# Performance work log

Hardware: AMD Instinct MI355X
Metric: run time of the kernel (lower is better)

The kernel has to match this reference:

```python
import jax, jax.numpy as jnp
import numpy as np

B = 64            # batch of graphs
E = 8978          # edge-simplices per graph (nodes of the Hodge-1 graph)
E2 = E // 2       # after Graclus pair-pooling
K = 4             # Laguerre polynomial order
DEG = 16          # avg degree of the (edge-)adjacency
SLOPE = 0.33      # LeakyReLU negative slope
EPS = 1e-5        # BatchNorm eps


def _make_edges(rng, b, n, deg):
    # block-diagonal batched edge list: each graph only connects within itself
    offs = np.repeat(np.arange(b, dtype=np.int64) * n, n * deg)
    dst = np.tile(np.repeat(np.arange(n, dtype=np.int64), deg), b) + offs
    src = rng.integers(0, n, size=b * n * deg) + offs
    return np.stack([src, dst]).astype(np.int32)


def setup_inputs() -> dict:
    rng = np.random.default_rng(0)
    ks = jax.random.split(jax.random.key(0), 12)
    N1 = B * E
    ei1 = _make_edges(rng, B, E, DEG)
    ei2 = _make_edges(rng, B, E2, DEG)
    return {
        "x_s": jax.random.normal(ks[0], (N1, 1), jnp.float32),
        "edge_index_s": jnp.asarray(ei1),
        "edge_weight_s": jax.random.uniform(ks[1], (ei1.shape[1],), jnp.float32) * (2.0 / DEG),
        "edge_index_s1": jnp.asarray(ei2),
        "edge_weight_s1": jax.random.uniform(ks[2], (ei2.shape[1],), jnp.float32) * (2.0 / DEG),
        "W0": jax.random.normal(ks[3], (K, 1, 32), jnp.float32) * 0.3,
        "b0": jnp.zeros((32,), jnp.float32),
        "g0": jnp.ones((32,), jnp.float32),
        "be0": jnp.zeros((32,), jnp.float32),
        "W1": jax.random.normal(ks[4], (K, 32, 32), jnp.float32) * 0.1,
        "b1": jnp.zeros((32,), jnp.float32),
        "g1": jnp.ones((32,), jnp.float32),
        "be1": jnp.zeros((32,), jnp.float32),
        "W2": jax.random.normal(ks[5], (K, 32, 1), jnp.float32) * 0.1,
        "b2": jnp.zeros((1,), jnp.float32),
        "g2": jnp.ones((1,), jnp.float32),
        "be2": jnp.zeros((1,), jnp.float32),
        "lin1_W": jax.random.normal(ks[6], (E2, 256), jnp.float32) * 0.02,
        "lin1_b": jnp.zeros((256,), jnp.float32),
        "bn1_g": jnp.ones((256,), jnp.float32),
        "bn1_b": jnp.zeros((256,), jnp.float32),
        "lin2_W": jax.random.normal(ks[7], (256, 128), jnp.float32) * 0.06,
        "lin2_b": jnp.zeros((128,), jnp.float32),
        "bn2_g": jnp.ones((128,), jnp.float32),
        "bn2_b": jnp.zeros((128,), jnp.float32),
        "lin3_W": jax.random.normal(ks[8], (128, 1), jnp.float32) * 0.09,
        "lin3_b": jnp.zeros((1,), jnp.float32),
    }


def _laguerre_layer(x, src, dst, ew, W, b, gamma, beta, n):
    """HodgeLaguerreConv (K-order Laguerre recurrence over sparse L) + BatchNorm + LeakyReLU."""
    def matvec(v):  # (L v)[i] = sum_j w_ij v[j]
        return jax.ops.segment_sum(ew[:, None] * v[src], dst, num_segments=n)
    Tp = x                      # L_0(L) x = x
    out = Tp @ W[0]
    Tc = x - matvec(x)          # L_1(L) x = x - L x
    out = out + Tc @ W[1]
    for k in range(1, K - 1):   # L_{k+1} = ((2k+1-L) L_k - k L_{k-1}) / (k+1)
        Tn = ((2 * k + 1) * Tc - matvec(Tc) - k * Tp) / (k + 1)
        out = out + Tn @ W[k + 1]
        Tp, Tc = Tc, Tn
    out = out + b
    out = gamma * (out - out.mean(0)) * jax.lax.rsqrt(out.var(0) + EPS) + beta
    return jnp.where(out > 0, out, SLOPE * out)


def _bn(h, g, b):
    return g * (h - h.mean(0)) * jax.lax.rsqrt(h.var(0) + EPS) + b


def reference(x_s, edge_index_s, edge_weight_s, edge_index_s1, edge_weight_s1,
              W0, b0, g0, be0, W1, b1, g1, be1, W2, b2, g2, be2,
              lin1_W, lin1_b, bn1_g, bn1_b, lin2_W, lin2_b, bn2_g, bn2_b,
              lin3_W, lin3_b):
    N1, N2 = B * E, B * E2
    x = _laguerre_layer(x_s, edge_index_s[0], edge_index_s[1], edge_weight_s,
                        W0, b0, g0, be0, N1)
    # Graclus pooling: merge matched node pairs by max over features
    x = x.reshape(B, E2, 2, x.shape[-1]).max(axis=2).reshape(N2, -1)
    x = _laguerre_layer(x, edge_index_s1[0], edge_index_s1[1], edge_weight_s1,
                        W1, b1, g1, be1, N2)
    x = _laguerre_layer(x, edge_index_s1[0], edge_index_s1[1], edge_weight_s1,
                        W2, b2, g2, be2, N2)
    x = x.reshape(B, E2)        # last conv has 1 channel
    h = jax.nn.relu(_bn(x @ lin1_W + lin1_b, bn1_g, bn1_b))
    h = jax.nn.relu(_bn(h @ lin2_W + lin2_b, bn2_g, bn2_b))
    return h @ lin3_W + lin3_b  # [B, num_classes=1]
```

## Files before the change

kernel.cpp:

```cpp
#include <hip/hip_runtime.h>
#include <cstdint>

#define SLOPE 0.33f

static constexpr int B_   = 64;
static constexpr int E1_  = 8978;
static constexpr int E2_  = 4489;
static constexpr int N1_  = B_ * E1_;
static constexpr int N2_  = B_ * E2_;
static constexpr int DEG_ = 16;
static constexpr int QTR_ = 2245;
static constexpr int QTR2_ = 1123;
static constexpr int MVGRID = (N2_ * 32) / 256;
static constexpr int PROJ_GRID = (N2_ + 511) / 512;
static constexpr double EPS_ = 1e-5;

__device__ __forceinline__ float lrelu(float v) { return v > 0.f ? v : SLOPE * v; }
__device__ __forceinline__ float dot4(float4 a, float4 b) {
  return a.x * b.x + a.y * b.y + a.z * b.z + a.w * b.w;
}

__global__ __launch_bounds__(1024) void k0_chain(const float* __restrict__ x,
    const int* __restrict__ src, const float* __restrict__ ew,
    float* __restrict__ T1, float* __restrict__ T2, float* __restrict__ T3,
    double* mom) {
  __shared__ float sx[E1_], s1[E1_], s2[E1_];
  __shared__ double sred[16][14];
  int v = (blockIdx.x & 7) * 32 + (blockIdx.x >> 3);
  int g = v >> 2, q = v & 3;
  int gbase = g * E1_;
  int tid = threadIdx.x;
  for (int i = tid; i < E1_; i += 1024) sx[i] = x[gbase + i];
  __syncthreads();
  for (int i = tid; i < E1_; i += 1024) {
    const int4* s4 = (const int4*)(src + (size_t)(gbase + i) * DEG_);
    const float4* w4 = (const float4*)(ew + (size_t)(gbase + i) * DEG_);
    float acc = 0.f;
#pragma unroll
    for (int j = 0; j < 4; ++j) {
      int4 s = s4[j]; float4 w = w4[j];
      acc += w.x * sx[s.x - gbase] + w.y * sx[s.y - gbase]
           + w.z * sx[s.z - gbase] + w.w * sx[s.w - gbase];
    }
    s1[i] = sx[i] - acc;
  }
  __syncthreads();
  for (int i = tid; i < E1_; i += 1024) {
    const int4* s4 = (const int4*)(src + (size_t)(gbase + i) * DEG_);
    const float4* w4 = (const float4*)(ew + (size_t)(gbase + i) * DEG_);
    float acc = 0.f;
#pragma unroll
    for (int j = 0; j < 4; ++j) {
      int4 s = s4[j]; float4 w = w4[j];
      acc += w.x * s1[s.x - gbase] + w.y * s1[s.y - gbase]
           + w.z * s1[s.z - gbase] + w.w * s1[s.w - gbase];
    }
    s2[i] = (3.f * s1[i] - acc - sx[i]) * 0.5f;
  }
  __syncthreads();
  double m[14];
#pragma unroll
  for (int j = 0; j < 14; ++j) m[j] = 0.0;
  int start = q * QTR_, end = min(start + QTR_, E1_);
  for (int i = start + tid; i < end; i += 1024) {
    const int4* s4 = (const int4*)(src + (size_t)(gbase + i) * DEG_);
    const float4* w4 = (const float4*)(ew + (size_t)(gbase + i) * DEG_);
    float acc = 0.f;
#pragma unroll
    for (int j = 0; j < 4; ++j) {
      int4 s = s4[j]; float4 w = w4[j];
      acc += w.x * s2[s.x - gbase] + w.y * s2[s.y - gbase]
           + w.z * s2[s.z - gbase] + w.w * s2[s.w - gbase];
    }
    float t1 = s1[i], t2 = s2[i];
    float t3 = (5.f * t2 - acc - 2.f * t1) * (1.f / 3.f);
    T1[gbase + i] = t1;
    T2[gbase + i] = t2;
    T3[gbase + i] = t3;
    double d0 = sx[i], d1 = t1, d2 = t2, d3 = t3;
    m[0] += d0; m[1] += d1; m[2] += d2; m[3] += d3;
    m[4] += d0 * d0; m[5] += d0 * d1; m[6] += d0 * d2; m[7] += d0 * d3;
    m[8] += d1 * d1; m[9] += d1 * d2; m[10] += d1 * d3;
    m[11] += d2 * d2; m[12] += d2 * d3; m[13] += d3 * d3;
  }
  int lane = tid & 63, wid = tid >> 6;
#pragma unroll
  for (int j = 0; j < 14; ++j) {
    double vv = m[j];
    for (int o = 32; o; o >>= 1) vv += __shfl_down(vv, o);
    if (lane == 0) sred[wid][j] = vv;
  }
  __syncthreads();
  if (tid < 14) {
    double s = 0.0;
#pragma unroll
    for (int w = 0; w < 16; ++w) s += sred[w][tid];
    atomicAdd(&mom[tid], s);
  }
}

__global__ void k0_params(const double* __restrict__ mom, const float* __restrict__ W0,
    const float* __restrict__ g0, const float* __restrict__ be0,
    float* __restrict__ scale0, float* __restrict__ shiftE0) {
  int c = threadIdx.x;
  if (c >= 32) return;
  double inv = 1.0 / (double)N1_;
  double mm[4];
#pragma unroll
  for (int k = 0; k < 4; ++k) mm[k] = mom[k] * inv;
  double M[4][4];
  M[0][0] = mom[4] * inv;  M[0][1] = mom[5] * inv;  M[0][2] = mom[6] * inv;  M[0][3] = mom[7] * inv;
  M[1][1] = mom[8] * inv;  M[1][2] = mom[9] * inv;  M[1][3] = mom[10] * inv;
  M[2][2] = mom[11] * inv; M[2][3] = mom[12] * inv; M[3][3] = mom[13] * inv;
  M[1][0] = M[0][1]; M[2][0] = M[0][2]; M[3][0] = M[0][3];
  M[2][1] = M[1][2]; M[3][1] = M[1][3]; M[3][2] = M[2][3];
  double w[4];
#pragma unroll
  for (int k = 0; k < 4; ++k) w[k] = W0[k * 32 + c];
  double mean = 0.0;
#pragma unroll
  for (int k = 0; k < 4; ++k) mean += w[k] * mm[k];
  double e2 = 0.0;
#pragma unroll
  for (int k = 0; k < 4; ++k)
#pragma unroll
    for (int l = 0; l < 4; ++l) e2 += M[k][l] * w[k] * w[l];
  double var = e2 - mean * mean;
  double sc = (double)g0[c] / sqrt(var + EPS_);
  scale0[c] = (float)sc;
  shiftE0[c] = (float)((double)be0[c] - sc * mean);
}

__global__ __launch_bounds__(256) void k0_pool(const float* __restrict__ x,
    const float* __restrict__ T1, const float* __restrict__ T2, const float* __restrict__ T3,
    const float* __restrict__ W0, const float* __restrict__ scale0,
    const float* __restrict__ shiftE0, float* __restrict__ x1) {
  int gid = blockIdx.x * 256 + threadIdx.x;
  int grp = gid >> 5, c = gid & 31;
  if (grp >= N2_) return;
  int b = grp / E2_, j = grp - b * E2_;
  int ga = b * E1_ + 2 * j, gb = ga + 1;
  float w0 = W0[c], w1 = W0[32 + c], w2 = W0[64 + c], w3 = W0[96 + c];
  float da = x[ga] * w0 + T1[ga] * w1 + T2[ga] * w2 + T3[ga] * w3;
  float db = x[gb] * w0 + T1[gb] * w1 + T2[gb] * w2 + T3[gb] * w3;
  float sc = scale0[c], sh = shiftE0[c];
  float ya = lrelu(sc * da + sh), yb = lrelu(sc * db + sh);
  x1[grp * 32 + c] = fmaxf(ya, yb);
}

__global__ __launch_bounds__(256) void k1_projall(const float* __restrict__ X,
    const float* __restrict__ W1, float4* __restrict__ P4) {
  __shared__ float4 Wl[128 * 8];
  const float4 cfs[4] = { {0.f, 0.f, 0.f, -1.f / 6.f},
                          {0.f, 0.f, 0.5f, 1.5f},
                          {0.f, -1.f, -2.f, -3.f},
                          {1.f, 1.f, 1.f, 1.f} };
  for (int e = threadIdx.x; e < 1024; e += 256) {
    int o = e >> 3, qq = e & 7;
    int j = o >> 5, cp = o & 31;
    float4 cf = cfs[j];
    float4 w;
    {
      const float* wp = W1 + (4 * qq + 0) * 32 + cp;
      w.x = cf.x * wp[0] + cf.y * wp[1024] + cf.z * wp[2048] + cf.w * wp[3072];
    }
    {
      const float* wp = W1 + (4 * qq + 1) * 32 + cp;
      w.y = cf.x * wp[0] + cf.y * wp[1024] + cf.z * wp[2048] + cf.w * wp[3072];
    }
    {
      const float* wp = W1 + (4 * qq + 2) * 32 + cp;
      w.z = cf.x * wp[0] + cf.y * wp[1024] + cf.z * wp[2048] + cf.w * wp[3072];
    }
    {
      const float* wp = W1 + (4 * qq + 3) * 32 + cp;
      w.w = cf.x * wp[0] + cf.y * wp[1024] + cf.z * wp[2048] + cf.w * wp[3072];
    }
    Wl[e] = w;
  }
  __syncthreads();
  int rA = blockIdx.x * 512 + threadIdx.x;
  int rB = rA + 256;
  bool okA = rA < N2_, okB = rB < N2_;
  if (!okA) return;
  float4 xA[8], xB[8];
  {
    const float4* pa = (const float4*)(X + (size_t)rA * 32);
#pragma unroll
    for (int t = 0; t < 8; ++t) xA[t] = pa[t];
  }
  if (okB) {
    const float4* pb = (const float4*)(X + (size_t)rB * 32);
#pragma unroll
    for (int t = 0; t < 8; ++t) xB[t] = pb[t];
  } else {
#pragma unroll
    for (int t = 0; t < 8; ++t) xB[t] = {0.f, 0.f, 0.f, 0.f};
  }
  for (int oq = 0; oq < 32; ++oq) {
    float4 aA = {0.f, 0.f, 0.f, 0.f}, aB = {0.f, 0.f, 0.f, 0.f};
    const float4* wr = Wl + oq * 32;
#pragma unroll
    for (int qq = 0; qq < 8; ++qq) {
      float4 w0 = wr[0 * 8 + qq];
      float4 w1 = wr[1 * 8 + qq];
      float4 w2 = wr[2 * 8 + qq];
      float4 w3 = wr[3 * 8 + qq];
      float4 xa = xA[qq], xb = xB[qq];
      aA.x += dot4(xa, w0); aA.y += dot4(xa, w1); aA.z += dot4(xa, w2); aA.w += dot4(xa, w3);
      aB.x += dot4(xb, w0); aB.y += dot4(xb, w1); aB.z += dot4(xb, w2); aB.w += dot4(xb, w3);
    }
    P4[(size_t)oq * N2_ + rA] = aA;
    if (okB) P4[(size_t)oq * N2_ + rB] = aB;
  }
}

__global__ __launch_bounds__(1024) void k1_chain(const float4* __restrict__ P4,
    float4* __restrict__ O4, const int* __restrict__ src,
    const float* __restrict__ ew, double* st) {
  __shared__ float4 bA[E2_], bB[E2_];
  __shared__ float sacc[8];
  int v = (blockIdx.x & 7) * 64 + (blockIdx.x >> 3);
  int g = v >> 3, cg = v & 7;
  int gbase = g * E2_;
  int tid = threadIdx.x;
  if (tid < 8) sacc[tid] = 0.f;
  {
    const float4* sp = P4 + (size_t)cg * N2_ + gbase;
    for (int i = tid; i < E2_; i += 1024) bA[i] = sp[i];
  }
  float4* cur = bA;
  float4* nxt = bB;
  for (int s = 1; s <= 3; ++s) {
    __syncthreads();
    const float4* selfp = P4 + (size_t)(s * 8 + cg) * N2_ + gbase;
    for (int n = tid; n < E2_; n += 1024) {
      const int4* s4 = (const int4*)(src + (size_t)(gbase + n) * DEG_);
      const float4* w4 = (const float4*)(ew + (size_t)(gbase + n) * DEG_);
      float4 acc = selfp[n];
#pragma unroll
      for (int j = 0; j < 4; ++j) {
        int4 sx = s4[j]; float4 w = w4[j];
        float4 g0 = cur[sx.x - gbase];
        float4 g1 = cur[sx.y - gbase];
        float4 g2 = cur[sx.z - gbase];
        float4 g3 = cur[sx.w - gbase];
        acc.x += w.x * g0.x + w.y * g1.x + w.z * g2.x + w.w * g3.x;
        acc.y += w.x * g0.y + w.y * g1.y + w.z * g2.y + w.w * g3.y;
        acc.z += w.x * g0.z + w.y * g1.z + w.z * g2.z + w.w * g3.z;
        acc.w += w.x * g0.w + w.y * g1.w + w.z * g2.w + w.w * g3.w;
      }
      nxt[n] = acc;
    }
    float4* t = cur; cur = nxt; nxt = t;
  }
  __syncthreads();
  float4* op = O4 + (size_t)cg * N2_ + gbase;
  float4 s1 = {0.f, 0.f, 0.f, 0.f}, s2 = {0.f, 0.f, 0.f, 0.f};
  for (int n = tid; n < E2_; n += 1024) {
    float4 vv = cur[n];
    op[n] = vv;
    s1.x += vv.x; s1.y += vv.y; s1.z += vv.z; s1.w += vv.w;
    s2.x += vv.x * vv.x; s2.y += vv.y * vv.y; s2.z += vv.z * vv.z; s2.w += vv.w * vv.w;
  }
  for (int o = 32; o; o >>= 1) {
    s1.x += __shfl_down(s1.x, o); s1.y += __shfl_down(s1.y, o);
    s1.z += __shfl_down(s1.z, o); s1.w += __shfl_down(s1.w, o);
    s2.x += __shfl_down(s2.x, o); s2.y += __shfl_down(s2.y, o);
    s2.z += __shfl_down(s2.z, o); s2.w += __shfl_down(s2.w, o);
  }
  if ((tid & 63) == 0) {
    atomicAdd(&sacc[0], s1.x); atomicAdd(&sacc[1], s1.y);
    atomicAdd(&sacc[2], s1.z); atomicAdd(&sacc[3], s1.w);
    atomicAdd(&sacc[4], s2.x); atomicAdd(&sacc[5], s2.y);
    atomicAdd(&sacc[6], s2.z); atomicAdd(&sacc[7], s2.w);
  }
  __syncthreads();
  if (tid < 4) {
    int ch = cg * 4 + tid;
    atomicAdd(&st[ch], (double)sacc[tid]);
    atomicAdd(&st[32 + ch], (double)sacc[4 + tid]);
  }
}

__global__ void k1_params(const double* __restrict__ sum, const double* __restrict__ sq,
    const float* __restrict__ g1, const float* __restrict__ be1,
    float* __restrict__ scale1, float* __restrict__ shiftE1) {
  int c = threadIdx.x;
  if (c >= 32) return;
  double mean = sum[c] / (double)N2_;
  double var = sq[c] / (double)N2_ - mean * mean;
  double sc = (double)g1[c] / sqrt(var + EPS_);
  scale1[c] = (float)sc;
  shiftE1[c] = (float)((double)be1[c] - sc * mean);
}

__global__ __launch_bounds__(256) void k2_proj(const float* __restrict__ X,
    const float* __restrict__ W2, const float* __restrict__ scale1,
    const float* __restrict__ shiftE1,
    float* __restrict__ u0, float* __restrict__ u1,
    float* __restrict__ u2, float* __restrict__ u3) {
  __shared__ float qv[4][32];
  __shared__ float fsc[32], fsh[32];
  int tid = threadIdx.x;
  if (tid < 128) {
    int cp = tid & 31, j = tid >> 5;
    float w0 = W2[cp], w1 = W2[32 + cp], w2 = W2[64 + cp], w3 = W2[96 + cp];
    float q;
    if (j == 0)      q = w0 + w1 + w2 + w3;
    else if (j == 1) q = -w1 - 2.f * w2 - 3.f * w3;
    else if (j == 2) q = 0.5f * w2 + 1.5f * w3;
    else             q = -w3 * (1.f / 6.f);
    qv[j][cp] = q;
  }
  if (tid < 32) { fsc[tid] = scale1[tid]; fsh[tid] = shiftE1[tid]; }
  __syncthreads();
  int node = blockIdx.x * 256 + tid;
  if (node >= N2_) return;
  const float4* xf = (const float4*)X;
  float a0 = 0.f, a1 = 0.f, a2 = 0.f, a3 = 0.f;
#pragma unroll
  for (int t = 0; t < 8; ++t) {
    float4 v = xf[(size_t)t * N2_ + node];
    float f0 = lrelu(fsc[4 * t] * v.x + fsh[4 * t]);
    float f1 = lrelu(fsc[4 * t + 1] * v.y + fsh[4 * t + 1]);
    float f2_ = lrelu(fsc[4 * t + 2] * v.z + fsh[4 * t + 2]);
    float f3 = lrelu(fsc[4 * t + 3] * v.w + fsh[4 * t + 3]);
    a0 += f0 * qv[0][4 * t] + f1 * qv[0][4 * t + 1] + f2_ * qv[0][4 * t + 2] + f3 * qv[0][4 * t + 3];
    a1 += f0 * qv[1][4 * t] + f1 * qv[1][4 * t + 1] + f2_ * qv[1][4 * t + 2] + f3 * qv[1][4 * t + 3];
    a2 += f0 * qv[2][4 * t] + f1 * qv[2][4 * t + 1] + f2_ * qv[2][4 * t + 2] + f3 * qv[2][4 * t + 3];
    a3 += f0 * qv[3][4 * t] + f1 * qv[3][4 * t + 1] + f2_ * qv[3][4 * t + 2] + f3 * qv[3][4 * t + 3];
  }
  u0[node] = a0; u1[node] = a1; u2[node] = a2; u3[node] = a3;
}

__global__ __launch_bounds__(256) void k2_step(const float* __restrict__ z,
    const int* __restrict__ src, const float* __restrict__ ew,
    const float* __restrict__ u, float* __restrict__ zo,
    int do_stats, double* st2) {
  __shared__ float sz[E2_];
  __shared__ double sred[4][2];
  int g = blockIdx.x >> 2, q = blockIdx.x & 3;
  int gbase = g * E2_;
  for (int j = threadIdx.x; j < E2_; j += 256) sz[j] = z[gbase + j];
  __syncthreads();
  int start = q * QTR2_, end = min(start + QTR2_, E2_);
  double aS = 0.0, aQ = 0.0;
  for (int i = start + (int)threadIdx.x; i < end; i += 256) {
    int node = gbase + i;
    const int4* s4 = (const int4*)(src + (size_t)node * DEG_);
    const float4* w4 = (const float4*)(ew + (size_t)node * DEG_);
    float acc = 0.f;
#pragma unroll
    for (int j = 0; j < 4; ++j) {
      int4 s = s4[j]; float4 w = w4[j];
      acc += w.x * sz[s.x - gbase] + w.y * sz[s.y - gbase]
           + w.z * sz[s.z - gbase] + w.w * sz[s.w - gbase];
    }
    float val = u[node] + acc;
    zo[node] = val;
    if (do_stats) { aS += val; aQ += (double)val * (double)val; }
  }
  if (do_stats) {
    int lane = threadIdx.x & 63, wid = threadIdx.x >> 6;
    for (int o = 32; o; o >>= 1) { aS += __shfl_down(aS, o); aQ += __shfl_down(aQ, o); }
    if (lane == 0) { sred[wid][0] = aS; sred[wid][1] = aQ; }
    __syncthreads();
    if (threadIdx.x == 0) {
      double s = sred[0][0] + sred[1][0] + sred[2][0] + sred[3][0];
      double qq = sred[0][1] + sred[1][1] + sred[2][1] + sred[3][1];
      atomicAdd(&st2[0], s); atomicAdd(&st2[1], qq);
    }
  }
}

__global__ void k2_params(const double* __restrict__ st2, const float* __restrict__ g2,
    const float* __restrict__ be2, float* __restrict__ p ) {
  if (threadIdx.x != 0) return;
  double mean = st2[0] / (double)N2_;
  double var = st2[1] / (double)N2_ - mean * mean;
  double sc = (double)g2[0] / sqrt(var + EPS_);
  p[128] = (float)sc;
  p[129] = (float)((double)be2[0] - sc * mean);
}

__global__ __launch_bounds__(256) void k3_gemm1(const float* __restrict__ out2,
    const float* __restrict__ lin1W, const float* __restrict__ p, float* h1pre) {
  __shared__ float f2v[4][284];
  float sc = p[128], sh = p[129];
  int bs = blockIdx.x & 15, rs = blockIdx.x >> 4;
  int b0 = bs * 4;
  int r0 = rs * 281;
  int nr = min(281, E2_ - r0);
  int c = threadIdx.x;
#pragma unroll
  for (int b = 0; b < 4; ++b)
    for (int j = c; j < 284; j += 256)
      f2v[b][j] = (j < nr) ? lrelu(sc * out2[(b0 + b) * E2_ + r0 + j] + sh) : 0.f;
  __syncthreads();
  float acc0 = 0.f, acc1 = 0.f, acc2 = 0.f, acc3 = 0.f;
  int nr4 = nr & ~3;
  int j = 0;
  for (; j < nr4; j += 4) {
    const float* wp = lin1W + (size_t)(r0 + j) * 256 + c;
    float w0 = wp[0], w1 = wp[256], w2 = wp[512], w3 = wp[768];
    float4 f0 = *(const float4*)&f2v[0][j];
    float4 f1 = *(const float4*)&f2v[1][j];
    float4 f2_ = *(const float4*)&f2v[2][j];
    float4 f3 = *(const float4*)&f2v[3][j];
    acc0 += f0.x * w0 + f0.y * w1 + f0.z * w2 + f0.w * w3;
    acc1 += f1.x * w0 + f1.y * w1 + f1.z * w2 + f1.w * w3;
    acc2 += f2_.x * w0 + f2_.y * w1 + f2_.z * w2 + f2_.w * w3;
    acc3 += f3.x * w0 + f3.y * w1 + f3.z * w2 + f3.w * w3;
  }
  for (; j < nr; ++j) {
    float w = lin1W[(size_t)(r0 + j) * 256 + c];
    acc0 += f2v[0][j] * w;
    acc1 += f2v[1][j] * w;
    acc2 += f2v[2][j] * w;
    acc3 += f2v[3][j] * w;
  }
  atomicAdd(&h1pre[(b0 + 0) * 256 + c], acc0);
  atomicAdd(&h1pre[(b0 + 1) * 256 + c], acc1);
  atomicAdd(&h1pre[(b0 + 2) * 256 + c], acc2);
  atomicAdd(&h1pre[(b0 + 3) * 256 + c], acc3);
}

__global__ __launch_bounds__(256) void k4_bn1(const float* __restrict__ h1pre,
    const float* __restrict__ g, const float* __restrict__ be, float* __restrict__ h1) {
  int c = threadIdx.x;
  float vs[64];
  double s = 0.0, q = 0.0;
  for (int b = 0; b < 64; ++b) { float v = h1pre[b * 256 + c]; vs[b] = v; s += v; q += (double)v * v; }
  double mean = s / 64.0, var = q / 64.0 - mean * mean;
  double scd = (double)g[c] / sqrt(var + EPS_);
  double shd = (double)be[c] - scd * mean;
  for (int b = 0; b < 64; ++b) {
    float y = (float)(scd * vs[b] + shd);
    h1[b * 256 + c] = y > 0.f ? y : 0.f;
  }
}

__global__ __launch_bounds__(256) void k5_gemm2(const float* __restrict__ h1,
    const float* __restrict__ lin2W, float* __restrict__ h2pre) {
  __shared__ float sred[256];
  int c = blockIdx.x;
  int b = threadIdx.x & 63, q = threadIdx.x >> 6;
  float acc = 0.f;
  for (int r = q; r < 256; r += 4) acc += h1[b * 256 + r] * lin2W[r * 128 + c];
  sred[threadIdx.x] = acc;
  __syncthreads();
  if (threadIdx.x < 64)
    h2pre[threadIdx.x * 128 + c] = sred[threadIdx.x] + sred[64 + threadIdx.x]
                                 + sred[128 + threadIdx.x] + sred[192 + threadIdx.x];
}

__global__ __launch_bounds__(256) void k6_final(const float* __restrict__ h2pre,
    const float* __restrict__ g, const float* __restrict__ be,
    const float* __restrict__ W3, const float* __restrict__ b3, float* __restrict__ outp) {
  __shared__ float sh2[64 * 129];
  __shared__ float sred[256];
  int tid = threadIdx.x;
  if (tid < 128) {
    int c = tid;
    float vs[64];
    double s = 0.0, q = 0.0;
    for (int b = 0; b < 64; ++b) { float v = h2pre[b * 128 + c]; vs[b] = v; s += v; q += (double)v * v; }
    double mean = s / 64.0, var = q / 64.0 - mean * mean;
    double scd = (double)g[c] / sqrt(var + EPS_);
    double shd = (double)be[c] - scd * mean;
    for (int b = 0; b < 64; ++b) {
      float y = (float)(scd * vs[b] + shd);
      sh2[b * 129 + c] = y > 0.f ? y : 0.f;
    }
  }
  __syncthreads();
  int b = tid & 63, q = tid >> 6;
  float acc = 0.f;
  for (int r = q; r < 128; r += 4) acc += sh2[b * 129 + r] * W3[r];
  sred[tid] = acc;
  __syncthreads();
  if (tid < 64)
    outp[tid] = sred[tid] + sred[64 + tid] + sred[128 + tid] + sred[192 + tid] + b3[0];
}

extern "C" void kernel_launch(void* const* d_in, const int* in_sizes, int n_in,
                              void* d_out, int out_size, void* d_ws, size_t ws_size,
                              hipStream_t stream) {
  const float* x    = (const float*)d_in[0];
  const int*   ei1  = (const int*)d_in[1];
  const float* ew1  = (const float*)d_in[2];
  const int*   ei2  = (const int*)d_in[3];
  const float* ew2  = (const float*)d_in[4];
  const float* W0   = (const float*)d_in[5];
  const float* g0   = (const float*)d_in[7];
  const float* be0  = (const float*)d_in[8];
  const float* W1   = (const float*)d_in[9];
  const float* g1   = (const float*)d_in[11];
  const float* be1  = (const float*)d_in[12];
  const float* W2   = (const float*)d_in[13];
  const float* g2   = (const float*)d_in[15];
  const float* be2  = (const float*)d_in[16];
  const float* lin1W = (const float*)d_in[17];
  const float* bn1g = (const float*)d_in[19];
  const float* bn1b = (const float*)d_in[20];
  const float* lin2W = (const float*)d_in[21];
  const float* bn2g = (const float*)d_in[23];
  const float* bn2b = (const float*)d_in[24];
  const float* lin3W = (const float*)d_in[25];
  const float* lin3b = (const float*)d_in[26];

  char* ws = (char*)d_ws;
  double* stats  = (double*)ws;
  float*  params = (float*)(ws + 1024);
  float*  h1pre  = (float*)(ws + 4096);
  float*  h1     = (float*)(ws + 4096 + 65536);
  float*  h2pre  = (float*)(ws + 4096 + 131072);
  float*  Treg   = (float*)(ws + 262144);
  float* T1_0 = Treg;
  float* T2_0 = Treg + N1_;
  float* T3_0 = Treg + 2 * (size_t)N1_;
  float* u0   = Treg;
  float* u1   = Treg + (size_t)N2_;
  float* u2   = Treg + 2 * (size_t)N2_;
  float* u3   = Treg + 3 * (size_t)N2_;
  float* zA   = Treg + 4 * (size_t)N2_;
  float* out2 = Treg + 5 * (size_t)N2_;
  float*  big = (float*)(ws + 262144 + 3 * (size_t)N1_ * 4);
  float* bufA = big;
  float* Pbuf = big + 32 * (size_t)N2_;

  hipMemsetAsync(stats, 0, 80 * sizeof(double), stream);
  hipMemsetAsync(h1pre, 0, 65536, stream);

  k0_chain<<<256, 1024, 0, stream>>>(x, ei1, ew1, T1_0, T2_0, T3_0, stats);
  k0_params<<<1, 32, 0, stream>>>(stats, W0, g0, be0, params, params + 32);
  k0_pool<<<MVGRID, 256, 0, stream>>>(x, T1_0, T2_0, T3_0, W0, params, params + 32, bufA);

  k1_projall<<<PROJ_GRID, 256, 0, stream>>>(bufA, W1, (float4*)Pbuf);
  k1_chain<<<512, 1024, 0, stream>>>((const float4*)Pbuf, (float4*)Pbuf, ei2, ew2, stats + 14);
  k1_params<<<1, 32, 0, stream>>>(stats + 14, stats + 46, g1, be1, params + 64, params + 96);

  k2_proj<<<(N2_ + 255) / 256, 256, 0, stream>>>(Pbuf, W2, params + 64, params + 96,
                                                 u0, u1, u2, u3);
  k2_step<<<256, 256, 0, stream>>>(u3, ei2, ew2, u2, zA, 0, nullptr);
  k2_step<<<256, 256, 0, stream>>>(zA, ei2, ew2, u1, u3, 0, nullptr);
  k2_step<<<256, 256, 0, stream>>>(u3, ei2, ew2, u0, out2, 1, stats + 78);
  k2_params<<<1, 64, 0, stream>>>(stats + 78, g2, be2, params);

  k3_gemm1<<<256, 256, 0, stream>>>(out2, lin1W, params, h1pre);
  k4_bn1<<<1, 256, 0, stream>>>(h1pre, bn1g, bn1b, h1);
  k5_gemm2<<<128, 256, 0, stream>>>(h1, lin2W, h2pre);
  k6_final<<<1, 256, 0, stream>>>(h2pre, bn2g, bn2b, lin3W, lin3b, (float*)d_out);
}
```

Before: 542.1 us.

## Fuse pooling into projection, merge layer-2 steps, fold param kernels, fuse MLP head

```diff
diff --git a/kernel.cpp b/kernel.cpp
--- a/kernel.cpp
+++ b/kernel.cpp
@@ -11,7 +11,6 @@
 static constexpr int DEG_ = 16;
 static constexpr int QTR_ = 2245;
 static constexpr int QTR2_ = 1123;
-static constexpr int MVGRID = (N2_ * 32) / 256;
 static constexpr int PROJ_GRID = (N2_ + 511) / 512;
 static constexpr double EPS_ = 1e-5;
 
@@ -99,63 +98,50 @@
   }
 }
 
-__global__ void k0_params(const double* __restrict__ mom, const float* __restrict__ W0,
-    const float* __restrict__ g0, const float* __restrict__ be0,
-    float* __restrict__ scale0, float* __restrict__ shiftE0) {
-  int c = threadIdx.x;
-  if (c >= 32) return;
-  double inv = 1.0 / (double)N1_;
-  double mm[4];
-#pragma unroll
-  for (int k = 0; k < 4; ++k) mm[k] = mom[k] * inv;
-  double M[4][4];
-  M[0][0] = mom[4] * inv;  M[0][1] = mom[5] * inv;  M[0][2] = mom[6] * inv;  M[0][3] = mom[7] * inv;
-  M[1][1] = mom[8] * inv;  M[1][2] = mom[9] * inv;  M[1][3] = mom[10] * inv;
-  M[2][2] = mom[11] * inv; M[2][3] = mom[12] * inv; M[3][3] = mom[13] * inv;
-  M[1][0] = M[0][1]; M[2][0] = M[0][2]; M[3][0] = M[0][3];
-  M[2][1] = M[1][2]; M[3][1] = M[1][3]; M[3][2] = M[2][3];
-  double w[4];
-#pragma unroll
-  for (int k = 0; k < 4; ++k) w[k] = W0[k * 32 + c];
-  double mean = 0.0;
-#pragma unroll
-  for (int k = 0; k < 4; ++k) mean += w[k] * mm[k];
-  double e2 = 0.0;
-#pragma unroll
-  for (int k = 0; k < 4; ++k)
-#pragma unroll
-    for (int l = 0; l < 4; ++l) e2 += M[k][l] * w[k] * w[l];
-  double var = e2 - mean * mean;
-  double sc = (double)g0[c] / sqrt(var + EPS_);
-  scale0[c] = (float)sc;
-  shiftE0[c] = (float)((double)be0[c] - sc * mean);
-}
-
-__global__ __launch_bounds__(256) void k0_pool(const float* __restrict__ x,
-    const float* __restrict__ T1, const float* __restrict__ T2, const float* __restrict__ T3,
-    const float* __restrict__ W0, const float* __restrict__ scale0,
-    const float* __restrict__ shiftE0, float* __restrict__ x1) {
-  int gid = blockIdx.x * 256 + threadIdx.x;
-  int grp = gid >> 5, c = gid & 31;
-  if (grp >= N2_) return;
-  int b = grp / E2_, j = grp - b * E2_;
-  int ga = b * E1_ + 2 * j, gb = ga + 1;
-  float w0 = W0[c], w1 = W0[32 + c], w2 = W0[64 + c], w3 = W0[96 + c];
-  float da = x[ga] * w0 + T1[ga] * w1 + T2[ga] * w2 + T3[ga] * w3;
-  float db = x[gb] * w0 + T1[gb] * w1 + T2[gb] * w2 + T3[gb] * w3;
-  float sc = scale0[c], sh = shiftE0[c];
-  float ya = lrelu(sc * da + sh), yb = lrelu(sc * db + sh);
-  x1[grp * 32 + c] = fmaxf(ya, yb);
-}
-
-__global__ __launch_bounds__(256) void k1_projall(const float* __restrict__ X,
-    const float* __restrict__ W1, float4* __restrict__ P4) {
+__global__ __launch_bounds__(256) void k1_projpool(const float* __restrict__ x,
+    const float* __restrict__ T1, const float* __restrict__ T2,
+    const float* __restrict__ T3, const float* __restrict__ W0,
+    const double* __restrict__ mom, const float* __restrict__ g0,
+    const float* __restrict__ be0, const float* __restrict__ W1,
+    float4* __restrict__ P4) {
   __shared__ float4 Wl[128 * 8];
+  __shared__ float sW0[128];
+  __shared__ float sc0[32], sh0[32];
   const float4 cfs[4] = { {0.f, 0.f, 0.f, -1.f / 6.f},
                           {0.f, 0.f, 0.5f, 1.5f},
                           {0.f, -1.f, -2.f, -3.f},
                           {1.f, 1.f, 1.f, 1.f} };
-  for (int e = threadIdx.x; e < 1024; e += 256) {
+  int tid = threadIdx.x;
+  if (tid < 32) {
+    int c = tid;
+    double inv = 1.0 / (double)N1_;
+    double mm[4];
+#pragma unroll
+    for (int k = 0; k < 4; ++k) mm[k] = mom[k] * inv;
+    double M[4][4];
+    M[0][0] = mom[4] * inv;  M[0][1] = mom[5] * inv;  M[0][2] = mom[6] * inv;  M[0][3] = mom[7] * inv;
+    M[1][1] = mom[8] * inv;  M[1][2] = mom[9] * inv;  M[1][3] = mom[10] * inv;
+    M[2][2] = mom[11] * inv; M[2][3] = mom[12] * inv; M[3][3] = mom[13] * inv;
+    M[1][0] = M[0][1]; M[2][0] = M[0][2]; M[3][0] = M[0][3];
+    M[2][1] = M[1][2]; M[3][1] = M[1][3]; M[3][2] = M[2][3];
+    double w[4];
+#pragma unroll
+    for (int k = 0; k < 4; ++k) w[k] = W0[k * 32 + c];
+    double mean = 0.0;
+#pragma unroll
+    for (int k = 0; k < 4; ++k) mean += w[k] * mm[k];
+    double e2 = 0.0;
+#pragma unroll
+    for (int k = 0; k < 4; ++k)
+#pragma unroll
+      for (int l = 0; l < 4; ++l) e2 += M[k][l] * w[k] * w[l];
+    double var = e2 - mean * mean;
+    double sc = (double)g0[c] / sqrt(var + EPS_);
+    sc0[c] = (float)sc;
+    sh0[c] = (float)((double)be0[c] - sc * mean);
+  }
+  for (int e = tid; e < 128; e += 256) sW0[e] = W0[e];
+  for (int e = tid; e < 1024; e += 256) {
     int o = e >> 3, qq = e & 7;
     int j = o >> 5, cp = o & 31;
     float4 cf = cfs[j];
@@ -179,20 +165,54 @@
     Wl[e] = w;
   }
   __syncthreads();
-  int rA = blockIdx.x * 512 + threadIdx.x;
+  int rA = blockIdx.x * 512 + tid;
   int rB = rA + 256;
   bool okA = rA < N2_, okB = rB < N2_;
   if (!okA) return;
   float4 xA[8], xB[8];
   {
-    const float4* pa = (const float4*)(X + (size_t)rA * 32);
-#pragma unroll
-    for (int t = 0; t < 8; ++t) xA[t] = pa[t];
+    int b = rA / E2_, j = rA - b * E2_;
+    int ga = b * E1_ + 2 * j;
+    float2 xv = *(const float2*)(x + ga);
+    float2 t1v = *(const float2*)(T1 + ga);
+    float2 t2v = *(const float2*)(T2 + ga);
+    float2 t3v = *(const float2*)(T3 + ga);
+#pragma unroll
+    for (int t = 0; t < 8; ++t) {
+      float r[4];
+#pragma unroll
+      for (int k = 0; k < 4; ++k) {
+        int c = 4 * t + k;
+        float w0 = sW0[c], w1 = sW0[32 + c], w2 = sW0[64 + c], w3 = sW0[96 + c];
+        float da = xv.x * w0 + t1v.x * w1 + t2v.x * w2 + t3v.x * w3;
+        float db = xv.y * w0 + t1v.y * w1 + t2v.y * w2 + t3v.y * w3;
+        float s = sc0[c], h = sh0[c];
+        r[k] = fmaxf(lrelu(s * da + h), lrelu(s * db + h));
+      }
+      xA[t] = {r[0], r[1], r[2], r[3]};
+    }
   }
   if (okB) {
-    const float4* pb = (const float4*)(X + (size_t)rB * 32);
-#pragma unroll
-    for (int t = 0; t < 8; ++t) xB[t] = pb[t];
+    int b = rB / E2_, j = rB - b * E2_;
+    int ga = b * E1_ + 2 * j;
+    float2 xv = *(const float2*)(x + ga);
+    float2 t1v = *(const float2*)(T1 + ga);
+    float2 t2v = *(const float2*)(T2 + ga);
+    float2 t3v = *(const float2*)(T3 + ga);
+#pragma unroll
+    for (int t = 0; t < 8; ++t) {
+      float r[4];
+#pragma unroll
+      for (int k = 0; k < 4; ++k) {
+        int c = 4 * t + k;
+        float w0 = sW0[c], w1 = sW0[32 + c], w2 = sW0[64 + c], w3 = sW0[96 + c];
+        float da = xv.x * w0 + t1v.x * w1 + t2v.x * w2 + t3v.x * w3;
+        float db = xv.y * w0 + t1v.y * w1 + t2v.y * w2 + t3v.y * w3;
+        float s = sc0[c], h = sh0[c];
+        r[k] = fmaxf(lrelu(s * da + h), lrelu(s * db + h));
+      }
+      xB[t] = {r[0], r[1], r[2], r[3]};
+    }
   } else {
 #pragma unroll
     for (int t = 0; t < 8; ++t) xB[t] = {0.f, 0.f, 0.f, 0.f};
@@ -283,21 +303,10 @@
   }
 }
 
-__global__ void k1_params(const double* __restrict__ sum, const double* __restrict__ sq,
-    const float* __restrict__ g1, const float* __restrict__ be1,
-    float* __restrict__ scale1, float* __restrict__ shiftE1) {
-  int c = threadIdx.x;
-  if (c >= 32) return;
-  double mean = sum[c] / (double)N2_;
-  double var = sq[c] / (double)N2_ - mean * mean;
-  double sc = (double)g1[c] / sqrt(var + EPS_);
-  scale1[c] = (float)sc;
-  shiftE1[c] = (float)((double)be1[c] - sc * mean);
-}
-
 __global__ __launch_bounds__(256) void k2_proj(const float* __restrict__ X,
-    const float* __restrict__ W2, const float* __restrict__ scale1,
-    const float* __restrict__ shiftE1,
+    const float* __restrict__ W2, const double* __restrict__ sum,
+    const double* __restrict__ sq, const float* __restrict__ g1,
+    const float* __restrict__ be1,
     float* __restrict__ u0, float* __restrict__ u1,
     float* __restrict__ u2, float* __restrict__ u3) {
   __shared__ float qv[4][32];
@@ -313,7 +322,14 @@
     else             q = -w3 * (1.f / 6.f);
     qv[j][cp] = q;
   }
-  if (tid < 32) { fsc[tid] = scale1[tid]; fsh[tid] = shiftE1[tid]; }
+  if (tid < 32) {
+    int c = tid;
+    double mean = sum[c] / (double)N2_;
+    double var = sq[c] / (double)N2_ - mean * mean;
+    double sc = (double)g1[c] / sqrt(var + EPS_);
+    fsc[c] = (float)sc;
+    fsh[c] = (float)((double)be1[c] - sc * mean);
+  }
   __syncthreads();
   int node = blockIdx.x * 256 + tid;
   if (node >= N2_) return;
@@ -334,60 +350,80 @@
   u0[node] = a0; u1[node] = a1; u2[node] = a2; u3[node] = a3;
 }
 
-__global__ __launch_bounds__(256) void k2_step(const float* __restrict__ z,
-    const int* __restrict__ src, const float* __restrict__ ew,
-    const float* __restrict__ u, float* __restrict__ zo,
-    int do_stats, double* st2) {
-  __shared__ float sz[E2_];
+__global__ __launch_bounds__(256) void k2_chain(const float* __restrict__ u0,
+    const float* __restrict__ u1, const float* __restrict__ u2,
+    const float* __restrict__ u3, const int* __restrict__ src,
+    const float* __restrict__ ew, float* __restrict__ out2, double* st2) {
+  __shared__ float sA[E2_], sB[E2_];
   __shared__ double sred[4][2];
-  int g = blockIdx.x >> 2, q = blockIdx.x & 3;
+  int v = (blockIdx.x & 7) * 32 + (blockIdx.x >> 3);
+  int g = v >> 2, q = v & 3;
   int gbase = g * E2_;
-  for (int j = threadIdx.x; j < E2_; j += 256) sz[j] = z[gbase + j];
+  int tid = threadIdx.x;
+  for (int i = tid; i < E2_; i += 256) sA[i] = u3[gbase + i];
+  __syncthreads();
+  for (int i = tid; i < E2_; i += 256) {
+    const int4* s4 = (const int4*)(src + (size_t)(gbase + i) * DEG_);
+    const float4* w4 = (const float4*)(ew + (size_t)(gbase + i) * DEG_);
+    float acc = 0.f;
+#pragma unroll
+    for (int j = 0; j < 4; ++j) {
+      int4 s = s4[j]; float4 w = w4[j];
+      acc += w.x * sA[s.x - gbase] + w.y * sA[s.y - gbase]
+           + w.z * sA[s.z - gbase] + w.w * sA[s.w - gbase];
+    }
+    sB[i] = u2[gbase + i] + acc;
+  }
+  __syncthreads();
+  for (int i = tid; i < E2_; i += 256) {
+    const int4* s4 = (const int4*)(src + (size_t)(gbase + i) * DEG_);
+    const float4* w4 = (const float4*)(ew + (size_t)(gbase + i) * DEG_);
+    float acc = 0.f;
+#pragma unroll
+    for (int j = 0; j < 4; ++j) {
+      int4 s = s4[j]; float4 w = w4[j];
+      acc += w.x * sB[s.x - gbase] + w.y * sB[s.y - gbase]
+           + w.z * sB[s.z - gbase] + w.w * sB[s.w - gbase];
+    }
+    sA[i] = u1[gbase + i] + acc;
+  }
   __syncthreads();
   int start = q * QTR2_, end = min(start + QTR2_, E2_);
   double aS = 0.0, aQ = 0.0;
-  for (int i = start + (int)threadIdx.x; i < end; i += 256) {
-    int node = gbase + i;
-    const int4* s4 = (const int4*)(src + (size_t)node * DEG_);
-    const float4* w4 = (const float4*)(ew + (size_t)node * DEG_);
+  for (int i = start + tid; i < end; i += 256) {
+    const int4* s4 = (const int4*)(src + (size_t)(gbase + i) * DEG_);
+    const float4* w4 = (const float4*)(ew + (size_t)(gbase + i) * DEG_);
     float acc = 0.f;
 #pragma unroll
     for (int j = 0; j < 4; ++j) {
       int4 s = s4[j]; float4 w = w4[j];
-      acc += w.x * sz[s.x - gbase] + w.y * sz[s.y - gbase]
-           + w.z * sz[s.z - gbase] + w.w * sz[s.w - gbase];
-    }
-    float val = u[node] + acc;
-    zo[node] = val;
-    if (do_stats) { aS += val; aQ += (double)val * (double)val; }
-  }
-  if (do_stats) {
-    int lane = threadIdx.x & 63, wid = threadIdx.x >> 6;
-    for (int o = 32; o; o >>= 1) { aS += __shfl_down(aS, o); aQ += __shfl_down(aQ, o); }
-    if (lane == 0) { sred[wid][0] = aS; sred[wid][1] = aQ; }
-    __syncthreads();
-    if (threadIdx.x == 0) {
-      double s = sred[0][0] + sred[1][0] + sred[2][0] + sred[3][0];
-      double qq = sred[0][1] + sred[1][1] + sred[2][1] + sred[3][1];
-      atomicAdd(&st2[0], s); atomicAdd(&st2[1], qq);
-    }
-  }
-}
-
-__global__ void k2_params(const double* __restrict__ st2, const float* __restrict__ g2,
-    const float* __restrict__ be2, float* __restrict__ p ) {
-  if (threadIdx.x != 0) return;
+      acc += w.x * sA[s.x - gbase] + w.y * sA[s.y - gbase]
+           + w.z * sA[s.z - gbase] + w.w * sA[s.w - gbase];
+    }
+    float val = u0[gbase + i] + acc;
+    out2[gbase + i] = val;
+    aS += val; aQ += (double)val * (double)val;
+  }
+  int lane = tid & 63, wid = tid >> 6;
+  for (int o = 32; o; o >>= 1) { aS += __shfl_down(aS, o); aQ += __shfl_down(aQ, o); }
+  if (lane == 0) { sred[wid][0] = aS; sred[wid][1] = aQ; }
+  __syncthreads();
+  if (tid == 0) {
+    double s = sred[0][0] + sred[1][0] + sred[2][0] + sred[3][0];
+    double qq = sred[0][1] + sred[1][1] + sred[2][1] + sred[3][1];
+    atomicAdd(&st2[0], s); atomicAdd(&st2[1], qq);
+  }
+}
+
+__global__ __launch_bounds__(256) void k3_gemm1(const float* __restrict__ out2,
+    const float* __restrict__ lin1W, const double* __restrict__ st2,
+    const float* __restrict__ g2, const float* __restrict__ be2, float* h1pre) {
+  __shared__ float f2v[4][284];
   double mean = st2[0] / (double)N2_;
   double var = st2[1] / (double)N2_ - mean * mean;
-  double sc = (double)g2[0] / sqrt(var + EPS_);
-  p[128] = (float)sc;
-  p[129] = (float)((double)be2[0] - sc * mean);
-}
-
-__global__ __launch_bounds__(256) void k3_gemm1(const float* __restrict__ out2,
-    const float* __restrict__ lin1W, const float* __restrict__ p, float* h1pre) {
-  __shared__ float f2v[4][284];
-  float sc = p[128], sh = p[129];
+  double scd = (double)g2[0] / sqrt(var + EPS_);
+  float sc = (float)scd;
+  float sh = (float)((double)be2[0] - scd * mean);
   int bs = blockIdx.x & 15, rs = blockIdx.x >> 4;
   int b0 = bs * 4;
   int r0 = rs * 281;
@@ -426,62 +462,63 @@
   atomicAdd(&h1pre[(b0 + 3) * 256 + c], acc3);
 }
 
-__global__ __launch_bounds__(256) void k4_bn1(const float* __restrict__ h1pre,
-    const float* __restrict__ g, const float* __restrict__ be, float* __restrict__ h1) {
-  int c = threadIdx.x;
-  float vs[64];
-  double s = 0.0, q = 0.0;
-  for (int b = 0; b < 64; ++b) { float v = h1pre[b * 256 + c]; vs[b] = v; s += v; q += (double)v * v; }
-  double mean = s / 64.0, var = q / 64.0 - mean * mean;
-  double scd = (double)g[c] / sqrt(var + EPS_);
-  double shd = (double)be[c] - scd * mean;
-  for (int b = 0; b < 64; ++b) {
-    float y = (float)(scd * vs[b] + shd);
-    h1[b * 256 + c] = y > 0.f ? y : 0.f;
-  }
-}
-
-__global__ __launch_bounds__(256) void k5_gemm2(const float* __restrict__ h1,
-    const float* __restrict__ lin2W, float* __restrict__ h2pre) {
-  __shared__ float sred[256];
-  int c = blockIdx.x;
-  int b = threadIdx.x & 63, q = threadIdx.x >> 6;
-  float acc = 0.f;
-  for (int r = q; r < 256; r += 4) acc += h1[b * 256 + r] * lin2W[r * 128 + c];
-  sred[threadIdx.x] = acc;
-  __syncthreads();
-  if (threadIdx.x < 64)
-    h2pre[threadIdx.x * 128 + c] = sred[threadIdx.x] + sred[64 + threadIdx.x]
-                                 + sred[128 + threadIdx.x] + sred[192 + threadIdx.x];
-}
-
-__global__ __launch_bounds__(256) void k6_final(const float* __restrict__ h2pre,
-    const float* __restrict__ g, const float* __restrict__ be,
-    const float* __restrict__ W3, const float* __restrict__ b3, float* __restrict__ outp) {
+__global__ __launch_bounds__(1024) void k_head(const float* __restrict__ h1pre,
+    const float* __restrict__ bn1g, const float* __restrict__ bn1b,
+    const float* __restrict__ lin2W, const float* __restrict__ bn2g,
+    const float* __restrict__ bn2b, const float* __restrict__ W3,
+    const float* __restrict__ b3, float* __restrict__ outp) {
+  __shared__ float sh1[64 * 257];
   __shared__ float sh2[64 * 129];
-  __shared__ float sred[256];
   int tid = threadIdx.x;
+  if (tid < 256) {
+    int c = tid;
+    float vs[64];
+    double s = 0.0, q = 0.0;
+#pragma unroll
+    for (int b = 0; b < 64; ++b) { float v = h1pre[b * 256 + c]; vs[b] = v; s += v; q += (double)v * v; }
+    double mean = s / 64.0, var = q / 64.0 - mean * mean;
+    double scd = (double)bn1g[c] / sqrt(var + EPS_);
+    double shd = (double)bn1b[c] - scd * mean;
+#pragma unroll
+    for (int b = 0; b < 64; ++b) {
+      float y = (float)(scd * vs[b] + shd);
+      sh1[b * 257 + c] = y > 0.f ? y : 0.f;
+    }
+  }
+  __syncthreads();
+  {
+    int c = tid & 127, bg = tid >> 7;
+#pragma unroll
+    for (int bb = 0; bb < 8; ++bb) {
+      int b = bg * 8 + bb;
+      float acc = 0.f;
+      for (int r = 0; r < 256; ++r) acc += sh1[b * 257 + r] * lin2W[r * 128 + c];
+      sh2[b * 129 + c] = acc;
+    }
+  }
+  __syncthreads();
   if (tid < 128) {
     int c = tid;
     float vs[64];
     double s = 0.0, q = 0.0;
-    for (int b = 0; b < 64; ++b) { float v = h2pre[b * 128 + c]; vs[b] = v; s += v; q += (double)v * v; }
+#pragma unroll
+    for (int b = 0; b < 64; ++b) { float v = sh2[b * 129 + c]; vs[b] = v; s += v; q += (double)v * v; }
     double mean = s / 64.0, var = q / 64.0 - mean * mean;
-    double scd = (double)g[c] / sqrt(var + EPS_);
-    double shd = (double)be[c] - scd * mean;
+    double scd = (double)bn2g[c] / sqrt(var + EPS_);
+    double shd = (double)bn2b[c] - scd * mean;
+#pragma unroll
     for (int b = 0; b < 64; ++b) {
       float y = (float)(scd * vs[b] + shd);
       sh2[b * 129 + c] = y > 0.f ? y : 0.f;
     }
   }
   __syncthreads();
-  int b = tid & 63, q = tid >> 6;
-  float acc = 0.f;
-  for (int r = q; r < 128; r += 4) acc += sh2[b * 129 + r] * W3[r];
-  sred[tid] = acc;
-  __syncthreads();
-  if (tid < 64)
-    outp[tid] = sred[tid] + sred[64 + tid] + sred[128 + tid] + sred[192 + tid] + b3[0];
+  if (tid < 64) {
+    int b = tid;
+    float acc = b3[0];
+    for (int r = 0; r < 128; ++r) acc += sh2[b * 129 + r] * W3[r];
+    outp[b] = acc;
+  }
 }
 
 extern "C" void kernel_launch(void* const* d_in, const int* in_sizes, int n_in,
@@ -512,10 +549,7 @@
 
   char* ws = (char*)d_ws;
   double* stats  = (double*)ws;
-  float*  params = (float*)(ws + 1024);
   float*  h1pre  = (float*)(ws + 4096);
-  float*  h1     = (float*)(ws + 4096 + 65536);
-  float*  h2pre  = (float*)(ws + 4096 + 131072);
   float*  Treg   = (float*)(ws + 262144);
   float* T1_0 = Treg;
   float* T2_0 = Treg + N1_;
@@ -524,32 +558,24 @@
   float* u1   = Treg + (size_t)N2_;
   float* u2   = Treg + 2 * (size_t)N2_;
   float* u3   = Treg + 3 * (size_t)N2_;
-  float* zA   = Treg + 4 * (size_t)N2_;
-  float* out2 = Treg + 5 * (size_t)N2_;
+  float* out2 = Treg + 4 * (size_t)N2_;
   float*  big = (float*)(ws + 262144 + 3 * (size_t)N1_ * 4);
-  float* bufA = big;
-  float* Pbuf = big + 32 * (size_t)N2_;
+  float* Pbuf = big;
 
   hipMemsetAsync(stats, 0, 80 * sizeof(double), stream);
   hipMemsetAsync(h1pre, 0, 65536, stream);
 
   k0_chain<<<256, 1024, 0, stream>>>(x, ei1, ew1, T1_0, T2_0, T3_0, stats);
-  k0_params<<<1, 32, 0, stream>>>(stats, W0, g0, be0, params, params + 32);
-  k0_pool<<<MVGRID, 256, 0, stream>>>(x, T1_0, T2_0, T3_0, W0, params, params + 32, bufA);
-
-  k1_projall<<<PROJ_GRID, 256, 0, stream>>>(bufA, W1, (float4*)Pbuf);
+
+  k1_projpool<<<PROJ_GRID, 256, 0, stream>>>(x, T1_0, T2_0, T3_0, W0, stats, g0, be0,
+                                             W1, (float4*)Pbuf);
   k1_chain<<<512, 1024, 0, stream>>>((const float4*)Pbuf, (float4*)Pbuf, ei2, ew2, stats + 14);
-  k1_params<<<1, 32, 0, stream>>>(stats + 14, stats + 46, g1, be1, params + 64, params + 96);
-
-  k2_proj<<<(N2_ + 255) / 256, 256, 0, stream>>>(Pbuf, W2, params + 64, params + 96,
-                                                 u0, u1, u2, u3);
-  k2_step<<<256, 256, 0, stream>>>(u3, ei2, ew2, u2, zA, 0, nullptr);
-  k2_step<<<256, 256, 0, stream>>>(zA, ei2, ew2, u1, u3, 0, nullptr);
-  k2_step<<<256, 256, 0, stream>>>(u3, ei2, ew2, u0, out2, 1, stats + 78);
-  k2_params<<<1, 64, 0, stream>>>(stats + 78, g2, be2, params);
-
-  k3_gemm1<<<256, 256, 0, stream>>>(out2, lin1W, params, h1pre);
-  k4_bn1<<<1, 256, 0, stream>>>(h1pre, bn1g, bn1b, h1);
-  k5_gemm2<<<128, 256, 0, stream>>>(h1, lin2W, h2pre);
-  k6_final<<<1, 256, 0, stream>>>(h2pre, bn2g, bn2b, lin3W, lin3b, (float*)d_out);
-}
+
+  k2_proj<<<(N2_ + 255) / 256, 256, 0, stream>>>(Pbuf, W2, stats + 14, stats + 46,
+                                                 g1, be1, u0, u1, u2, u3);
+  k2_chain<<<256, 256, 0, stream>>>(u0, u1, u2, u3, ei2, ew2, out2, stats + 78);
+
+  k3_gemm1<<<256, 256, 0, stream>>>(out2, lin1W, stats + 78, g2, be2, h1pre);
+  k_head<<<1, 1024, 0, stream>>>(h1pre, bn1g, bn1b, lin2W, bn2g, bn2b, lin3W, lin3b,
+                                 (float*)d_out);
+}
```

Result: slower. 586.3 us (+8.1%).
